# Kernel tuning notes

Measured on AMD Instinct MI355X. Metric: run time of the kernel, lower is better.

## Reference

```python
import jax, jax.numpy as jnp
import numpy as np

B, C, L = 4, 256, 4096
C8 = C // 8

def setup_inputs() -> dict:
    key = jax.random.key(0)
    ks = jax.random.split(key, 8)
    s = 1.0 / np.sqrt(C)
    x = jax.random.normal(ks[0], (B, C, L), dtype=jnp.float32)
    Wq = jax.random.normal(ks[1], (C8, C), dtype=jnp.float32) * s
    bq = jax.random.normal(ks[2], (C8,), dtype=jnp.float32) * s
    Wk = jax.random.normal(ks[3], (C8, C), dtype=jnp.float32) * s
    bk = jax.random.normal(ks[4], (C8,), dtype=jnp.float32) * s
    Wv = jax.random.normal(ks[5], (C, C), dtype=jnp.float32) * s
    bv = jax.random.normal(ks[6], (C,), dtype=jnp.float32) * s
    gamma = jax.random.normal(ks[7], (1,), dtype=jnp.float32) * 0.1
    return {"x": x, "Wq": Wq, "bq": bq, "Wk": Wk, "bk": bk, "Wv": Wv, "bv": bv, "gamma": gamma}

def reference(x, Wq, bq, Wk, bk, Wv, bv, gamma):
    # pointwise conv1d == channel matmul: [O,C] x [B,C,L] -> [B,O,L]
    q = jnp.einsum('oc,bcl->bol', Wq, x) + bq[None, :, None]   # [B, C8, L]
    k = jnp.einsum('oc,bcl->bol', Wk, x) + bk[None, :, None]   # [B, C8, L]
    v = jnp.einsum('oc,bcl->bol', Wv, x) + bv[None, :, None]   # [B, C,  L]
    # attention[b,i,j] = sum_c q[b,c,i] * k[b,c,j]
    attn = jnp.einsum('bci,bcj->bij', q, k)                    # [B, L, L]
    attn = jax.nn.softmax(attn, axis=-1)
    # out[b,c,i] = sum_j v[b,c,j] * attn[b,i,j]
    out = jnp.einsum('bcj,bij->bci', v, attn)                  # [B, C, L]
    return gamma * out + x
```

## Files before the change

### kernel.cpp

```cpp
#include <hip/hip_runtime.h>
#include <math.h>

#define BB 4
#define CC 256
#define LL 4096
#define DD 32
#define LOG2E 1.44269504088896f

typedef __attribute__((ext_vector_type(8))) short short8;
typedef __attribute__((ext_vector_type(4))) short short4v;
typedef __attribute__((ext_vector_type(4))) float f32x4;
typedef __attribute__((ext_vector_type(4))) unsigned int uint4v;
typedef __attribute__((ext_vector_type(2))) unsigned int uint2v;

#define BARRIER() asm volatile("s_waitcnt lgkmcnt(0)\n\ts_barrier" ::: "memory")

__device__ inline unsigned short f2bf(float f) {
  union { float f; unsigned u; } v; v.f = f;
  unsigned r = v.u + 0x7fffu + ((v.u >> 16) & 1u);
  return (unsigned short)(r >> 16);
}

__device__ inline float fast_exp2(float x) {
#if __has_builtin(__builtin_amdgcn_exp2f)
  return __builtin_amdgcn_exp2f(x);
#else
  return exp2f(x);
#endif
}

__device__ __host__ inline int sigma32(int p) {
  const int q4 = (p >> 3) & 3, u = p & 7;
  return 16 * (u >> 2) + 4 * q4 + (u & 3);
}

__global__ __launch_bounds__(256) void wprep_kernel(
    const float* __restrict__ Wq, const float* __restrict__ Wk, const float* __restrict__ Wv,
    unsigned short* __restrict__ wf)
{
  const int t = threadIdx.x;
  const int ot = blockIdx.x >> 1;
  const int rep = blockIdx.x & 1;
  const int lane = t & 63, cl = lane & 15, q4 = lane >> 4;
  const int ks = (t >> 6) + 4 * rep;
  const int o = ot * 16 + cl;
  const int c = ks * 32 + q4 * 8;
  const float* src = (o < 32) ? (Wq + o * CC) : (o < 64) ? (Wk + (o - 32) * CC)
                                              : (Wv + (o - 64) * CC);
  const float sc = (o < 32) ? LOG2E : 1.0f;
  unsigned short p[8];
  #pragma unroll
  for (int j = 0; j < 8; ++j) p[j] = f2bf(src[c + j] * sc);
  uint4v u;
  u.x = (unsigned)p[0] | ((unsigned)p[1] << 16);
  u.y = (unsigned)p[2] | ((unsigned)p[3] << 16);
  u.z = (unsigned)p[4] | ((unsigned)p[5] << 16);
  u.w = (unsigned)p[6] | ((unsigned)p[7] << 16);
  *(uint4v*)(wf + ((size_t)(ot * 8 + ks) * 64 + lane) * 8) = u;
}

__global__ __launch_bounds__(512, 4) void qkv_kernel(
    const float* __restrict__ x, const unsigned short* __restrict__ wf,
    const float* __restrict__ bq, const float* __restrict__ bk, const float* __restrict__ bv,
    unsigned short* __restrict__ qT, unsigned short* __restrict__ kT,
    unsigned short* __restrict__ vf)
{
  __shared__ union {
    float xl[32 * 261];
    struct {
      unsigned short qk[32 * 72];
      __align__(16) unsigned short v[256 * 40];
    } ep;
  } sm;

  const int t = threadIdx.x;
  const int lane = t & 63, cl = lane & 15, q4 = lane >> 4;
  const int blk = blockIdx.x;
  const int b  = (blk & 7) >> 1;
  const int it = ((blk >> 3) << 1) + (blk & 1);
  const int i0 = it * 32;

  {
    const int ln8 = t & 7;
    #pragma unroll
    for (int p = 0; p < 4; ++p) {
      const int c = (t >> 3) + 64 * p;
      const f32x4 v = *(const f32x4*)(x + ((size_t)(b * CC + c)) * LL + i0 + ln8 * 4);
      #pragma unroll
      for (int k = 0; k < 4; ++k) sm.xl[(ln8 * 4 + k) * 261 + c] = v[k];
    }
  }
  __syncthreads();

  const int wi = (t >> 6) & 1, wo = t >> 7;
  const f32x4 zero = {0.f, 0.f, 0.f, 0.f};
  f32x4 acc[5];
  #pragma unroll
  for (int u = 0; u < 5; ++u) acc[u] = zero;

  for (int ks = 0; ks < 8; ++ks) {
    unsigned short p[8];
    #pragma unroll
    for (int j = 0; j < 8; ++j)
      p[j] = f2bf(sm.xl[(16 * wi + cl) * 261 + ks * 32 + q4 * 8 + j]);
    union { short8 s; uint4v u; } bfr;
    bfr.u.x = (unsigned)p[0] | ((unsigned)p[1] << 16);
    bfr.u.y = (unsigned)p[2] | ((unsigned)p[3] << 16);
    bfr.u.z = (unsigned)p[4] | ((unsigned)p[5] << 16);
    bfr.u.w = (unsigned)p[6] | ((unsigned)p[7] << 16);
    #pragma unroll
    for (int u = 0; u < 5; ++u) {
      const short8 a = *(const short8*)(wf + ((size_t)((wo * 5 + u) * 8 + ks) * 64 + lane) * 8);
      acc[u] = __builtin_amdgcn_mfma_f32_16x16x32_bf16(a, bfr.s, acc[u], 0, 0, 0);
    }
  }
  __syncthreads();

  #pragma unroll
  for (int u = 0; u < 5; ++u) {
    const int g = wo * 5 + u;
    if (g < 4) {
      short4v pk;
      #pragma unroll
      for (int r = 0; r < 4; ++r) {
        const int o = 16 * g + 4 * q4 + r;
        const float v = acc[u][r] + ((o < 32) ? bq[o] * LOG2E : bk[o - 32]);
        pk[r] = (short)f2bf(v);
      }
      *(short4v*)&sm.ep.qk[(16 * wi + cl) * 72 + 16 * g + 4 * q4] = pk;
    } else {
      #pragma unroll
      for (int r = 0; r < 4; ++r) {
        const int ch = 16 * (g - 4) + 4 * q4 + r;
        sm.ep.v[ch * 40 + 16 * wi + cl] = f2bf(acc[u][r] + bv[ch]);
      }
    }
  }
  __syncthreads();

  if (t < 64) {
    const int i = t >> 1, which = t & 1;
    const int gi = i0 + i;
    const unsigned short* srcp = &sm.ep.qk[i * 72 + which * 32];
    uint4v d0 = *(const uint4v*)(srcp + 0);
    uint4v d1 = *(const uint4v*)(srcp + 8);
    uint4v d2 = *(const uint4v*)(srcp + 16);
    uint4v d3 = *(const uint4v*)(srcp + 24);
    unsigned short* dst;
    if (which == 0) {
      dst = qT + ((size_t)b * LL + gi) * DD;
    } else {
      const int row = (gi & ~31) + sigma32(gi & 31);
      dst = kT + ((size_t)b * LL + row) * DD;
    }
    *(uint4v*)dst = d0; *(uint4v*)(dst + 8) = d1;
    *(uint4v*)(dst + 16) = d2; *(uint4v*)(dst + 24) = d3;
  }
  const int kk = it & 1, jt = it >> 1;
  #pragma unroll
  for (int rep = 0; rep < 2; ++rep) {
    const int slot = t + 512 * rep;
    const int fl = slot >> 6, l2 = slot & 63;
    const int cl2 = l2 & 15, q42 = l2 >> 4;
    const int m4 = fl >> 2, mt = fl & 3;
    const int fg = 8 * m4 + 4 * kk + mt;
    const int ch = 64 * m4 + 16 * mt + cl2;
    const uint4v d = *(const uint4v*)&sm.ep.v[ch * 40 + q42 * 8];
    *(uint4v*)(vf + (((size_t)(b * 64 + jt)) * 32 + fg) * 512 + l2 * 8) = d;
  }
}

__global__ __launch_bounds__(768, 3) void attn_kernel(
    const unsigned short* __restrict__ qT, const unsigned short* __restrict__ kT,
    const unsigned short* __restrict__ vf, const float* __restrict__ x,
    const float* __restrict__ gamma_p, float* __restrict__ out)
{
  __shared__ __align__(16) unsigned short P[2][8][4][64][8];
  __shared__ float l_lds[8][4][64];

  const int t = threadIdx.x;
  const int w = t >> 6, lane = t & 63, cl = lane & 15, q4 = lane >> 4;
  const int blk = blockIdx.x;
  const int b  = (blk & 7) >> 1;
  const int it = ((blk >> 3) << 1) + (blk & 1);
  const int i0 = it * 64;
  const f32x4 zero = {0.f, 0.f, 0.f, 0.f};

  if (w < 8) {
    const int pw = w;
    short8 qa[4];
    #pragma unroll
    for (int nt = 0; nt < 4; ++nt)
      qa[nt] = *(const short8*)(qT + ((size_t)b * LL + i0 + 16 * nt + cl) * DD + q4 * 8);
    const unsigned short* kbase =
        kT + ((size_t)b * LL + 32 * pw + cl) * DD + q4 * 8;
    short8 kb0 = *(const short8*)kbase;
    short8 kb1 = *(const short8*)(kbase + (size_t)16 * DD);
    float l_r[4] = {0.f, 0.f, 0.f, 0.f};

    auto produce = [&](int ss, int buf) {
      f32x4 s0[4], s1[4];
      #pragma unroll
      for (int nt = 0; nt < 4; ++nt)
        s0[nt] = __builtin_amdgcn_mfma_f32_16x16x32_bf16(kb0, qa[nt], zero, 0, 0, 0);
      #pragma unroll
      for (int nt = 0; nt < 4; ++nt)
        s1[nt] = __builtin_amdgcn_mfma_f32_16x16x32_bf16(kb1, qa[nt], zero, 0, 0, 0);
      const int nss = (ss + 1) & 15;
      kb0 = *(const short8*)(kbase + (size_t)(nss * 256) * DD);
      kb1 = *(const short8*)(kbase + (size_t)(nss * 256 + 16) * DD);
      #pragma unroll
      for (int nt = 0; nt < 4; ++nt) {
        const float a0 = fast_exp2(s0[nt][0]);
        const float a1 = fast_exp2(s0[nt][1]);
        const float a2 = fast_exp2(s0[nt][2]);
        const float a3 = fast_exp2(s0[nt][3]);
        const float b0 = fast_exp2(s1[nt][0]);
        const float b1 = fast_exp2(s1[nt][1]);
        const float b2 = fast_exp2(s1[nt][2]);
        const float b3 = fast_exp2(s1[nt][3]);
        uint4v u;
        u.x = __builtin_amdgcn_perm(__float_as_uint(a1), __float_as_uint(a0), 0x07060302);
        u.y = __builtin_amdgcn_perm(__float_as_uint(a3), __float_as_uint(a2), 0x07060302);
        u.z = __builtin_amdgcn_perm(__float_as_uint(b1), __float_as_uint(b0), 0x07060302);
        u.w = __builtin_amdgcn_perm(__float_as_uint(b3), __float_as_uint(b2), 0x07060302);
        *(uint4v*)&P[buf][pw][nt][lane][0] = u;
        l_r[nt] += ((a0 + a1) + (a2 + a3)) + ((b0 + b1) + (b2 + b3));
      }
    };

    produce(0, 0);
    __syncthreads();
    for (int i = 0; i < 16; ++i) {
      if (i < 15) produce(i + 1, (i + 1) & 1);
      BARRIER();
    }
    #pragma unroll
    for (int nt = 0; nt < 4; ++nt)
      l_lds[pw][nt][lane] = l_r[nt];
    BARRIER();
  } else {
    const int mq = w - 8;
    const unsigned short* vroot = vf + ((size_t)(b * 64)) * 32 * 512 + lane * 8;
    f32x4 O[4][4];
    #pragma unroll
    for (int j = 0; j < 4; ++j)
      #pragma unroll
      for (int nt = 0; nt < 4; ++nt) O[j][nt] = zero;

    short8 va[2][4];
    #pragma unroll
    for (int s = 0; s < 2; ++s) {
      const int g = s;
      const size_t base = ((size_t)(g >> 1) * 32 + 8 * mq + 4 * (g & 1)) * 512;
      #pragma unroll
      for (int j = 0; j < 4; ++j)
        va[s][j] = *(const short8*)(vroot + base + j * 512);
    }
    __syncthreads();

    for (int i = 0; i < 16; ++i) {
      const int buf = i & 1;
      short8 pb[2][4];
      #pragma unroll
      for (int nt = 0; nt < 4; ++nt)
        pb[0][nt] = *(const short8*)&P[buf][0][nt][lane][0];
      #pragma unroll
      for (int e = 0; e < 8; ++e) {
        const int cs = e & 1;
        if (e < 7) {
          #pragma unroll
          for (int nt = 0; nt < 4; ++nt)
            pb[cs ^ 1][nt] = *(const short8*)&P[buf][e + 1][nt][lane][0];
        }
        __builtin_amdgcn_s_setprio(1);
        #pragma unroll
        for (int j = 0; j < 4; ++j)
          #pragma unroll
          for (int nt = 0; nt < 4; ++nt)
            O[j][nt] = __builtin_amdgcn_mfma_f32_16x16x32_bf16(va[e & 1][j], pb[cs][nt],
                                                               O[j][nt], 0, 0, 0);
        __builtin_amdgcn_s_setprio(0);
        const int g2 = (8 * i + e + 2) & 127;
        const size_t base = ((size_t)(g2 >> 1) * 32 + 8 * mq + 4 * (g2 & 1)) * 512;
        #pragma unroll
        for (int j = 0; j < 4; ++j)
          va[e & 1][j] = *(const short8*)(vroot + base + j * 512);
      }
      BARRIER();
    }
    BARRIER();

    const float gam = gamma_p[0];
    float inv_l[4];
    #pragma unroll
    for (int nt = 0; nt < 4; ++nt) {
      float s = 0.f;
      #pragma unroll
      for (int pw = 0; pw < 8; ++pw)
        #pragma unroll
        for (int g = 0; g < 4; ++g)
          s += l_lds[pw][nt][g * 16 + cl];
      inv_l[nt] = 1.0f / s;
    }
    #pragma unroll
    for (int j = 0; j < 4; ++j) {
      #pragma unroll
      for (int nt = 0; nt < 4; ++nt) {
        #pragma unroll
        for (int r = 0; r < 4; ++r) {
          const int ch = 64 * mq + 16 * j + 4 * q4 + r;
          const int i  = i0 + 16 * nt + cl;
          const size_t idx = ((size_t)b * CC + ch) * LL + i;
          out[idx] = gam * O[j][nt][r] * inv_l[nt] + x[idx];
        }
      }
    }
  }
}

extern "C" void kernel_launch(void* const* d_in, const int* in_sizes, int n_in,
                              void* d_out, int out_size, void* d_ws, size_t ws_size,
                              hipStream_t stream) {
  const float* x     = (const float*)d_in[0];
  const float* Wq    = (const float*)d_in[1];
  const float* bq    = (const float*)d_in[2];
  const float* Wk    = (const float*)d_in[3];
  const float* bk    = (const float*)d_in[4];
  const float* Wv    = (const float*)d_in[5];
  const float* bv    = (const float*)d_in[6];
  const float* gamma = (const float*)d_in[7];
  float* out = (float*)d_out;

  unsigned short* qT = (unsigned short*)d_ws;
  unsigned short* kT = qT + (size_t)BB * LL * DD;
  unsigned short* vf = kT + (size_t)BB * LL * DD;
  unsigned short* wf = (unsigned short*)d_out;

  wprep_kernel<<<40, 256, 0, stream>>>(Wq, Wk, Wv, wf);
  qkv_kernel<<<512, 512, 0, stream>>>(x, wf, bq, bk, bv, qT, kT, vf);
  attn_kernel<<<256, 768, 0, stream>>>(qT, kT, vf, x, gamma, out);
}
```

Before: 131.6 us.

## Switch attention to 32x32x16 MFMA with fragment-ordered Q/K/V layouts

Replaces the 16x16x32 bf16 MFMA tiles in both the score and PV stages with 32x32x16 MFMA. The QKV kernel now writes Q, K and V directly in 32x32 fragment order so the attention kernel can load operands with single vector loads. P is packed to bf16 with v_cvt_pk_bf16_f32 and rearranged with v_permlane32_swap so its LDS layout matches the B operand of the PV MFMA. The aim is fewer MFMA issues and cheaper packing, at the cost of larger accumulators (more VGPR pressure) and a changed LDS and output indexing scheme.

```diff
diff --git a/kernel.cpp b/kernel.cpp
--- a/kernel.cpp
+++ b/kernel.cpp
@@ -10,6 +10,7 @@
 typedef __attribute__((ext_vector_type(8))) short short8;
 typedef __attribute__((ext_vector_type(4))) short short4v;
 typedef __attribute__((ext_vector_type(4))) float f32x4;
+typedef __attribute__((ext_vector_type(16))) float f32x16;
 typedef __attribute__((ext_vector_type(4))) unsigned int uint4v;
 typedef __attribute__((ext_vector_type(2))) unsigned int uint2v;
 
@@ -27,11 +28,6 @@
 #else
   return exp2f(x);
 #endif
-}
-
-__device__ __host__ inline int sigma32(int p) {
-  const int q4 = (p >> 3) & 3, u = p & 7;
-  return 16 * (u >> 2) + 4 * q4 + (u & 3);
 }
 
 __global__ __launch_bounds__(256) void wprep_kernel(
@@ -62,8 +58,8 @@
 __global__ __launch_bounds__(512, 4) void qkv_kernel(
     const float* __restrict__ x, const unsigned short* __restrict__ wf,
     const float* __restrict__ bq, const float* __restrict__ bk, const float* __restrict__ bv,
-    unsigned short* __restrict__ qT, unsigned short* __restrict__ kT,
-    unsigned short* __restrict__ vf)
+    unsigned short* __restrict__ qF, unsigned short* __restrict__ kF,
+    unsigned short* __restrict__ vF)
 {
   __shared__ union {
     float xl[32 * 261];
@@ -138,94 +134,89 @@
   }
   __syncthreads();
 
-  if (t < 64) {
-    const int i = t >> 1, which = t & 1;
-    const int gi = i0 + i;
-    const unsigned short* srcp = &sm.ep.qk[i * 72 + which * 32];
-    uint4v d0 = *(const uint4v*)(srcp + 0);
-    uint4v d1 = *(const uint4v*)(srcp + 8);
-    uint4v d2 = *(const uint4v*)(srcp + 16);
-    uint4v d3 = *(const uint4v*)(srcp + 24);
-    unsigned short* dst;
-    if (which == 0) {
-      dst = qT + ((size_t)b * LL + gi) * DD;
-    } else {
-      const int row = (gi & ~31) + sigma32(gi & 31);
-      dst = kT + ((size_t)b * LL + row) * DD;
-    }
-    *(uint4v*)dst = d0; *(uint4v*)(dst + 8) = d1;
-    *(uint4v*)(dst + 16) = d2; *(uint4v*)(dst + 24) = d3;
-  }
-  const int kk = it & 1, jt = it >> 1;
+  if (t < 256) {
+    const int which = t >> 7;
+    const int c = (t >> 6) & 1;
+    const int l = t & 63, hi2 = l >> 5, ql2 = l & 31;
+    const uint4v d = *(const uint4v*)&sm.ep.qk[ql2 * 72 + which * 32 + c * 16 + hi2 * 8];
+    unsigned short* dstf = which ? kF : qF;
+    *(uint4v*)(dstf + (((size_t)(b * 128 + it) * 2 + c) * 64 + l) * 8) = d;
+  }
   #pragma unroll
   for (int rep = 0; rep < 2; ++rep) {
     const int slot = t + 512 * rep;
-    const int fl = slot >> 6, l2 = slot & 63;
-    const int cl2 = l2 & 15, q42 = l2 >> 4;
-    const int m4 = fl >> 2, mt = fl & 3;
-    const int fg = 8 * m4 + 4 * kk + mt;
-    const int ch = 64 * m4 + 16 * mt + cl2;
-    const uint4v d = *(const uint4v*)&sm.ep.v[ch * 40 + q42 * 8];
-    *(uint4v*)(vf + (((size_t)(b * 64 + jt)) * 32 + fg) * 512 + l2 * 8) = d;
+    const int fl = slot >> 6, l = slot & 63;
+    const int g = fl >> 3, m = fl & 7;
+    const int hi2 = l >> 5, cl2 = l & 31;
+    const uint4v d = *(const uint4v*)&sm.ep.v[(32 * m + cl2) * 40 + g * 16 + hi2 * 8];
+    *(uint4v*)(vF + (((size_t)(b * 256 + 2 * it + g) * 8 + m) * 64 + l) * 8) = d;
   }
 }
 
 __global__ __launch_bounds__(768, 3) void attn_kernel(
-    const unsigned short* __restrict__ qT, const unsigned short* __restrict__ kT,
-    const unsigned short* __restrict__ vf, const float* __restrict__ x,
+    const unsigned short* __restrict__ qF, const unsigned short* __restrict__ kF,
+    const unsigned short* __restrict__ vF, const float* __restrict__ x,
     const float* __restrict__ gamma_p, float* __restrict__ out)
 {
-  __shared__ __align__(16) unsigned short P[2][8][4][64][8];
-  __shared__ float l_lds[8][4][64];
+  __shared__ __align__(16) unsigned short P[2 * 8 * 2 * 2 * 512];
+  __shared__ float l_lds[8][2][64];
 
   const int t = threadIdx.x;
-  const int w = t >> 6, lane = t & 63, cl = lane & 15, q4 = lane >> 4;
+  const int w = t >> 6, lane = t & 63, ql = lane & 31, hi = lane >> 5;
   const int blk = blockIdx.x;
   const int b  = (blk & 7) >> 1;
   const int it = ((blk >> 3) << 1) + (blk & 1);
   const int i0 = it * 64;
-  const f32x4 zero = {0.f, 0.f, 0.f, 0.f};
 
   if (w < 8) {
     const int pw = w;
-    short8 qa[4];
-    #pragma unroll
-    for (int nt = 0; nt < 4; ++nt)
-      qa[nt] = *(const short8*)(qT + ((size_t)b * LL + i0 + 16 * nt + cl) * DD + q4 * 8);
-    const unsigned short* kbase =
-        kT + ((size_t)b * LL + 32 * pw + cl) * DD + q4 * 8;
-    short8 kb0 = *(const short8*)kbase;
-    short8 kb1 = *(const short8*)(kbase + (size_t)16 * DD);
-    float l_r[4] = {0.f, 0.f, 0.f, 0.f};
+    short8 qB[2][2];
+    #pragma unroll
+    for (int qt = 0; qt < 2; ++qt)
+      #pragma unroll
+      for (int c = 0; c < 2; ++c)
+        qB[qt][c] = *(const short8*)(qF +
+            (((size_t)(b * 128 + it * 2 + qt) * 2 + c) * 64 + lane) * 8);
+    short8 kA[2];
+    #pragma unroll
+    for (int c = 0; c < 2; ++c)
+      kA[c] = *(const short8*)(kF + (((size_t)(b * 128 + pw) * 2 + c) * 64 + lane) * 8);
+    float l_r[2] = {0.f, 0.f};
+    const f32x16 z16 = {0.f,0.f,0.f,0.f,0.f,0.f,0.f,0.f,0.f,0.f,0.f,0.f,0.f,0.f,0.f,0.f};
 
     auto produce = [&](int ss, int buf) {
-      f32x4 s0[4], s1[4];
-      #pragma unroll
-      for (int nt = 0; nt < 4; ++nt)
-        s0[nt] = __builtin_amdgcn_mfma_f32_16x16x32_bf16(kb0, qa[nt], zero, 0, 0, 0);
-      #pragma unroll
-      for (int nt = 0; nt < 4; ++nt)
-        s1[nt] = __builtin_amdgcn_mfma_f32_16x16x32_bf16(kb1, qa[nt], zero, 0, 0, 0);
-      const int nss = (ss + 1) & 15;
-      kb0 = *(const short8*)(kbase + (size_t)(nss * 256) * DD);
-      kb1 = *(const short8*)(kbase + (size_t)(nss * 256 + 16) * DD);
-      #pragma unroll
-      for (int nt = 0; nt < 4; ++nt) {
-        const float a0 = fast_exp2(s0[nt][0]);
-        const float a1 = fast_exp2(s0[nt][1]);
-        const float a2 = fast_exp2(s0[nt][2]);
-        const float a3 = fast_exp2(s0[nt][3]);
-        const float b0 = fast_exp2(s1[nt][0]);
-        const float b1 = fast_exp2(s1[nt][1]);
-        const float b2 = fast_exp2(s1[nt][2]);
-        const float b3 = fast_exp2(s1[nt][3]);
-        uint4v u;
-        u.x = __builtin_amdgcn_perm(__float_as_uint(a1), __float_as_uint(a0), 0x07060302);
-        u.y = __builtin_amdgcn_perm(__float_as_uint(a3), __float_as_uint(a2), 0x07060302);
-        u.z = __builtin_amdgcn_perm(__float_as_uint(b1), __float_as_uint(b0), 0x07060302);
-        u.w = __builtin_amdgcn_perm(__float_as_uint(b3), __float_as_uint(b2), 0x07060302);
-        *(uint4v*)&P[buf][pw][nt][lane][0] = u;
-        l_r[nt] += ((a0 + a1) + (a2 + a3)) + ((b0 + b1) + (b2 + b3));
+      f32x16 S[2];
+      __builtin_amdgcn_s_setprio(1);
+      #pragma unroll
+      for (int qt = 0; qt < 2; ++qt)
+        S[qt] = __builtin_amdgcn_mfma_f32_32x32x16_bf16(kA[0], qB[qt][0], z16, 0, 0, 0);
+      #pragma unroll
+      for (int qt = 0; qt < 2; ++qt)
+        S[qt] = __builtin_amdgcn_mfma_f32_32x32x16_bf16(kA[1], qB[qt][1], S[qt], 0, 0, 0);
+      __builtin_amdgcn_s_setprio(0);
+      const int ntile = ((ss + 1) & 15) * 8 + pw;
+      #pragma unroll
+      for (int c = 0; c < 2; ++c)
+        kA[c] = *(const short8*)(kF + (((size_t)(b * 128 + ntile) * 2 + c) * 64 + lane) * 8);
+      #pragma unroll
+      for (int qt = 0; qt < 2; ++qt) {
+        float ex[16];
+        #pragma unroll
+        for (int r = 0; r < 16; ++r) ex[r] = fast_exp2(S[qt][r]);
+        l_r[qt] += ((((ex[0] + ex[1]) + (ex[2] + ex[3])) + ((ex[4] + ex[5]) + (ex[6] + ex[7])))
+                 + (((ex[8] + ex[9]) + (ex[10] + ex[11])) + ((ex[12] + ex[13]) + (ex[14] + ex[15]))));
+        #pragma unroll
+        for (int c = 0; c < 2; ++c) {
+          unsigned w0, w1, w2, w3;
+          asm("v_cvt_pk_bf16_f32 %0, %1, %2" : "=v"(w0) : "v"(ex[8 * c + 0]), "v"(ex[8 * c + 1]));
+          asm("v_cvt_pk_bf16_f32 %0, %1, %2" : "=v"(w1) : "v"(ex[8 * c + 2]), "v"(ex[8 * c + 3]));
+          asm("v_cvt_pk_bf16_f32 %0, %1, %2" : "=v"(w2) : "v"(ex[8 * c + 4]), "v"(ex[8 * c + 5]));
+          asm("v_cvt_pk_bf16_f32 %0, %1, %2" : "=v"(w3) : "v"(ex[8 * c + 6]), "v"(ex[8 * c + 7]));
+          asm("v_permlane32_swap_b32 %0, %1" : "+v"(w0), "+v"(w2));
+          asm("v_permlane32_swap_b32 %0, %1" : "+v"(w1), "+v"(w3));
+          uint4v u; u.x = w0; u.y = w1; u.z = w2; u.w = w3;
+          *(uint4v*)(&P[(((buf * 8 + pw) * 2 + qt) * 2 + c) * 512 + hi * 256 + ql * 8]) = u;
+        }
       }
     };
 
@@ -235,87 +226,84 @@
       if (i < 15) produce(i + 1, (i + 1) & 1);
       BARRIER();
     }
-    #pragma unroll
-    for (int nt = 0; nt < 4; ++nt)
-      l_lds[pw][nt][lane] = l_r[nt];
+    l_lds[pw][0][lane] = l_r[0];
+    l_lds[pw][1][lane] = l_r[1];
     BARRIER();
   } else {
     const int mq = w - 8;
-    const unsigned short* vroot = vf + ((size_t)(b * 64)) * 32 * 512 + lane * 8;
-    f32x4 O[4][4];
-    #pragma unroll
-    for (int j = 0; j < 4; ++j)
-      #pragma unroll
-      for (int nt = 0; nt < 4; ++nt) O[j][nt] = zero;
-
-    short8 va[2][4];
-    #pragma unroll
-    for (int s = 0; s < 2; ++s) {
-      const int g = s;
-      const size_t base = ((size_t)(g >> 1) * 32 + 8 * mq + 4 * (g & 1)) * 512;
-      #pragma unroll
-      for (int j = 0; j < 4; ++j)
-        va[s][j] = *(const short8*)(vroot + base + j * 512);
-    }
+    const unsigned short* vroot = vF + (size_t)b * (256 * 8 * 512) + lane * 8;
+    f32x16 O[2][2];
+    #pragma unroll
+    for (int mi = 0; mi < 2; ++mi)
+      #pragma unroll
+      for (int qt = 0; qt < 2; ++qt) {
+        const f32x16 z16 = {0.f,0.f,0.f,0.f,0.f,0.f,0.f,0.f,0.f,0.f,0.f,0.f,0.f,0.f,0.f,0.f};
+        O[mi][qt] = z16;
+      }
+    short8 vA[4][2];
+    #pragma unroll
+    for (int s = 0; s < 4; ++s)
+      #pragma unroll
+      for (int mi = 0; mi < 2; ++mi)
+        vA[s][mi] = *(const short8*)(vroot + ((size_t)(s * 8 + 2 * mq + mi)) * 512);
     __syncthreads();
 
+    short8 pb[3][2];
     for (int i = 0; i < 16; ++i) {
       const int buf = i & 1;
-      short8 pb[2][4];
-      #pragma unroll
-      for (int nt = 0; nt < 4; ++nt)
-        pb[0][nt] = *(const short8*)&P[buf][0][nt][lane][0];
-      #pragma unroll
-      for (int e = 0; e < 8; ++e) {
-        const int cs = e & 1;
-        if (e < 7) {
+      #pragma unroll
+      for (int s = 0; s < 2; ++s)
+        #pragma unroll
+        for (int qt = 0; qt < 2; ++qt)
+          pb[s][qt] = *(const short8*)(&P[((((buf * 8 + 0) * 2 + qt) * 2 + s) * 512)
+                                          + hi * 256 + ql * 8]);
+      #pragma unroll
+      for (int s = 0; s < 16; ++s) {
+        if (s < 14) {
+          const int ns = s + 2, kk = ns >> 1, c = ns & 1;
           #pragma unroll
-          for (int nt = 0; nt < 4; ++nt)
-            pb[cs ^ 1][nt] = *(const short8*)&P[buf][e + 1][nt][lane][0];
+          for (int qt = 0; qt < 2; ++qt)
+            pb[ns % 3][qt] = *(const short8*)(&P[((((buf * 8 + kk) * 2 + qt) * 2 + c) * 512)
+                                                 + hi * 256 + ql * 8]);
         }
         __builtin_amdgcn_s_setprio(1);
         #pragma unroll
-        for (int j = 0; j < 4; ++j)
+        for (int mi = 0; mi < 2; ++mi)
           #pragma unroll
-          for (int nt = 0; nt < 4; ++nt)
-            O[j][nt] = __builtin_amdgcn_mfma_f32_16x16x32_bf16(va[e & 1][j], pb[cs][nt],
-                                                               O[j][nt], 0, 0, 0);
+          for (int qt = 0; qt < 2; ++qt)
+            O[mi][qt] = __builtin_amdgcn_mfma_f32_32x32x16_bf16(vA[s & 3][mi], pb[s % 3][qt],
+                                                                O[mi][qt], 0, 0, 0);
         __builtin_amdgcn_s_setprio(0);
-        const int g2 = (8 * i + e + 2) & 127;
-        const size_t base = ((size_t)(g2 >> 1) * 32 + 8 * mq + 4 * (g2 & 1)) * 512;
-        #pragma unroll
-        for (int j = 0; j < 4; ++j)
-          va[e & 1][j] = *(const short8*)(vroot + base + j * 512);
+        const int kg = (i * 16 + s + 4) & 255;
+        #pragma unroll
+        for (int mi = 0; mi < 2; ++mi)
+          vA[s & 3][mi] = *(const short8*)(vroot + ((size_t)(kg * 8 + 2 * mq + mi)) * 512);
       }
       BARRIER();
     }
     BARRIER();
 
     const float gam = gamma_p[0];
-    float inv_l[4];
-    #pragma unroll
-    for (int nt = 0; nt < 4; ++nt) {
+    float inv_l[2];
+    #pragma unroll
+    for (int qt = 0; qt < 2; ++qt) {
       float s = 0.f;
       #pragma unroll
       for (int pw = 0; pw < 8; ++pw)
-        #pragma unroll
-        for (int g = 0; g < 4; ++g)
-          s += l_lds[pw][nt][g * 16 + cl];
-      inv_l[nt] = 1.0f / s;
-    }
-    #pragma unroll
-    for (int j = 0; j < 4; ++j) {
-      #pragma unroll
-      for (int nt = 0; nt < 4; ++nt) {
-        #pragma unroll
-        for (int r = 0; r < 4; ++r) {
-          const int ch = 64 * mq + 16 * j + 4 * q4 + r;
-          const int i  = i0 + 16 * nt + cl;
-          const size_t idx = ((size_t)b * CC + ch) * LL + i;
-          out[idx] = gam * O[j][nt][r] * inv_l[nt] + x[idx];
+        s += l_lds[pw][qt][ql] + l_lds[pw][qt][ql + 32];
+      inv_l[qt] = 1.0f / s;
+    }
+    #pragma unroll
+    for (int mi = 0; mi < 2; ++mi)
+      #pragma unroll
+      for (int qt = 0; qt < 2; ++qt)
+        #pragma unroll
+        for (int r = 0; r < 16; ++r) {
+          const int ch = 64 * mq + 32 * mi + (r & 3) + 8 * (r >> 2) + 4 * hi;
+          const int ii = i0 + 32 * qt + ql;
+          const size_t idx = ((size_t)b * CC + ch) * LL + ii;
+          out[idx] = gam * O[mi][qt][r] * inv_l[qt] + x[idx];
         }
-      }
-    }
   }
 }
 
@@ -332,12 +320,12 @@
   const float* gamma = (const float*)d_in[7];
   float* out = (float*)d_out;
 
-  unsigned short* qT = (unsigned short*)d_ws;
-  unsigned short* kT = qT + (size_t)BB * LL * DD;
-  unsigned short* vf = kT + (size_t)BB * LL * DD;
+  unsigned short* qF = (unsigned short*)d_ws;
+  unsigned short* kF = qF + (size_t)BB * LL * DD;
+  unsigned short* vF = kF + (size_t)BB * LL * DD;
   unsigned short* wf = (unsigned short*)d_out;
 
   wprep_kernel<<<40, 256, 0, stream>>>(Wq, Wk, Wv, wf);
-  qkv_kernel<<<512, 512, 0, stream>>>(x, wf, bq, bk, bv, qT, kT, vf);
-  attn_kernel<<<256, 768, 0, stream>>>(qT, kT, vf, x, gamma, out);
-}
+  qkv_kernel<<<512, 512, 0, stream>>>(x, wf, bq, bk, bv, qF, kF, vF);
+  attn_kernel<<<256, 768, 0, stream>>>(qF, kF, vF, x, gamma, out);
+}
```

Measured after the change: 133.6 us. About the same (+1.5%).
